# Performance work log

Measured on AMD Instinct MI355X. Metric: run time of the kernel, lower is better.

## Reference

```python
import jax, jax.numpy as jnp
import numpy as np

D_MODEL = 1024
NHEAD = 16
HEAD_DIM = D_MODEL // NHEAD


def setup_inputs() -> dict:
    key = jax.random.key(0)
    ks = jax.random.split(key, 11)
    B, S = 4, 2048
    s = 1.0 / np.sqrt(D_MODEL)
    return {
        "q": jax.random.normal(ks[0], (B, S, D_MODEL), jnp.float32),
        "k": jax.random.normal(ks[1], (B, S, D_MODEL), jnp.float32),
        "v": jax.random.normal(ks[2], (B, S, D_MODEL), jnp.float32),
        "Wq": jax.random.normal(ks[3], (D_MODEL, D_MODEL), jnp.float32) * s,
        "bq": jnp.zeros((D_MODEL,), jnp.float32),
        "Wk": jax.random.normal(ks[4], (D_MODEL, D_MODEL), jnp.float32) * s,
        "bk": jnp.zeros((D_MODEL,), jnp.float32),
        "Wv": jax.random.normal(ks[5], (D_MODEL, D_MODEL), jnp.float32) * s,
        "bv": jnp.zeros((D_MODEL,), jnp.float32),
        "Wo": jax.random.normal(ks[6], (D_MODEL, D_MODEL), jnp.float32) * s,
        "bo": jnp.zeros((D_MODEL,), jnp.float32),
    }


def reference(q, k, v, Wq, bq, Wk, bk, Wv, bv, Wo, bo):
    B, S, _ = q.shape
    H, Dh = NHEAD, HEAD_DIM

    def proj(x, W, b):  # nn.Linear: x @ W.T + b, then split heads -> [B,H,S,Dh]
        y = x @ W.T + b
        return y.reshape(B, S, H, Dh).transpose(0, 2, 1, 3)

    qh = proj(q, Wq, bq)
    kh = proj(k, Wk, bk)
    vh = proj(v, Wv, bv)

    scores = jnp.einsum("bhsd,bhtd->bhst", qh, kh) / jnp.sqrt(jnp.float32(Dh))
    attn = jax.nn.softmax(scores, axis=-1)
    out = jnp.einsum("bhst,bhtd->bhsd", attn, vh)  # [B,H,S,Dh]
    out = out.transpose(0, 2, 1, 3).reshape(B, S, H * Dh)
    return out @ Wo.T + bo
```

## Files before the change

### kernel.cpp

```cpp
#include <hip/hip_runtime.h>


typedef short bf16x8 __attribute__((ext_vector_type(8)));
typedef short bf16x4 __attribute__((ext_vector_type(4)));
typedef float f32x4 __attribute__((ext_vector_type(4)));
typedef float f32x16 __attribute__((ext_vector_type(16)));
typedef unsigned int u32x4 __attribute__((ext_vector_type(4)));

__device__ __forceinline__ short f2bf(float x) {
    union { float f; unsigned int u; } un; un.f = x;
    unsigned int u = un.u;
    return (short)(unsigned short)((u + 0x7fffu + ((u >> 16) & 1u)) >> 16);
}

__device__ __forceinline__ void gll16(const void* g, void* l) {
    __builtin_amdgcn_global_load_lds(
        (const __attribute__((address_space(1))) void*)g,
        (__attribute__((address_space(3))) void*)l, 16, 0, 0);
}

__device__ __forceinline__ void plswap(unsigned& a, unsigned& b) {
    asm("v_permlane32_swap_b32 %0, %1" : "+v"(a), "+v"(b));
}

struct CvtArgs { const float* s[4]; unsigned short* d[4]; int n4; };
__global__ __launch_bounds__(256) void cvt_bf16(CvtArgs ca) {
    const float* s = ca.s[blockIdx.y];
    unsigned short* d = ca.d[blockIdx.y];
    int i = blockIdx.x * blockDim.x + threadIdx.x;
    int stride = gridDim.x * blockDim.x;
    const float4* s4 = reinterpret_cast<const float4*>(s);
    bf16x4* d4 = reinterpret_cast<bf16x4*>(d);
    for (; i < ca.n4; i += stride) {
        float4 x = s4[i];
        bf16x4 y;
        y[0] = f2bf(x.x); y[1] = f2bf(x.y); y[2] = f2bf(x.z); y[3] = f2bf(x.w);
        d4[i] = y;
    }
}

__device__ __forceinline__ void gemm_core(const unsigned short* __restrict__ A,
                                          const unsigned short* __restrict__ W,
                                          const float* __restrict__ bias,
                                          float scale, void* __restrict__ out,
                                          int mode) {
    __shared__ unsigned short As[2][128 * 64];
    __shared__ unsigned short Bs[2][128 * 64];
    const int tid = threadIdx.x;
    const int m0 = blockIdx.y * 128, n0 = blockIdx.x * 128;
    const int wave = tid >> 6, lane = tid & 63;
    const int wm = (wave >> 1) * 64, wn = (wave & 1) * 64;
    const int l15 = lane & 15, quad = lane >> 4;
    const int srow = tid >> 3;
    const int scol = ((tid & 7) ^ (srow & 7)) * 8;
    const int cb = (l15 & 7);

    f32x4 acc[4][4] = {};

#pragma unroll
    for (int ro = 0; ro < 4; ++ro) {
        gll16(&A[(size_t)(m0 + ro * 32 + srow) * 1024 + scol], &As[0][ro * 2048 + tid * 8]);
        gll16(&W[(size_t)(n0 + ro * 32 + srow) * 1024 + scol], &Bs[0][ro * 2048 + tid * 8]);
    }
    __syncthreads();

    for (int kt = 0; kt < 16; ++kt) {
        const int cur = kt & 1;
        if (kt < 15) {
            const int k0 = (kt + 1) * 64;
#pragma unroll
            for (int ro = 0; ro < 4; ++ro) {
                gll16(&A[(size_t)(m0 + ro * 32 + srow) * 1024 + k0 + scol], &As[cur ^ 1][ro * 2048 + tid * 8]);
                gll16(&W[(size_t)(n0 + ro * 32 + srow) * 1024 + k0 + scol], &Bs[cur ^ 1][ro * 2048 + tid * 8]);
            }
        }
#pragma unroll
        for (int kk = 0; kk < 2; ++kk) {
            const int co = ((4 * kk + quad) ^ cb) * 8;
            bf16x8 a[4], b[4];
#pragma unroll
            for (int i = 0; i < 4; ++i)
                a[i] = *reinterpret_cast<bf16x8*>(&As[cur][(wm + i * 16 + l15) * 64 + co]);
#pragma unroll
            for (int j = 0; j < 4; ++j)
                b[j] = *reinterpret_cast<bf16x8*>(&Bs[cur][(wn + j * 16 + l15) * 64 + co]);
#pragma unroll
            for (int i = 0; i < 4; ++i)
#pragma unroll
                for (int j = 0; j < 4; ++j)
                    acc[i][j] = __builtin_amdgcn_mfma_f32_16x16x32_bf16(a[i], b[j], acc[i][j], 0, 0, 0);
        }
        __syncthreads();
    }

#pragma unroll
    for (int i = 0; i < 4; ++i) {
#pragma unroll
        for (int j = 0; j < 4; ++j) {
#pragma unroll
            for (int r = 0; r < 4; ++r) {
                int m = m0 + wm + i * 16 + quad * 4 + r;
                int n = n0 + wn + j * 16 + l15;
                float val = (acc[i][j][r] + bias[n]) * scale;
                if (mode == 0) {
                    reinterpret_cast<float*>(out)[(size_t)m * 1024 + n] = val;
                } else {
                    int b_ = m >> 11, s = m & 2047, h = n >> 6, d = n & 63;
                    size_t off = (mode == 1)
                                     ? ((size_t)((b_ * 16 + h) * 2048 + s) * 64 + d)
                                     : ((size_t)((b_ * 16 + h) * 64 + d) * 2048 + s);
                    reinterpret_cast<unsigned short*>(out)[off] = (unsigned short)f2bf(val);
                }
            }
        }
    }
}

struct QkvArgs {
    const unsigned short* A[3];
    const unsigned short* W[3];
    const float* bias[3];
    float scale[3];
    unsigned short* out[3];
    int mode[3];
};
__global__ __launch_bounds__(256) void gemm_qkv(QkvArgs ga) {
    int z = blockIdx.z;
    gemm_core(ga.A[z], ga.W[z], ga.bias[z], ga.scale[z], ga.out[z], ga.mode[z]);
}

__global__ __launch_bounds__(256) void gemm_wo(const unsigned short* __restrict__ A,
                                               const unsigned short* __restrict__ W,
                                               const float* __restrict__ bias,
                                               float* __restrict__ out) {
    gemm_core(A, W, bias, 1.0f, out, 0);
}


#define SOFTMAX_PV(MT, VBASE)                                                        \
    {                                                                                \
        float e[16];                                                                 \
        _Pragma("unroll")                                                            \
        for (int r = 0; r < 16; ++r) e[r] = __builtin_amdgcn_exp2f(sacc[MT][r]);     \
        lacc += ((e[0] + e[1]) + (e[2] + e[3])) + ((e[4] + e[5]) + (e[6] + e[7])) +  \
                ((e[8] + e[9]) + (e[10] + e[11])) + ((e[12] + e[13]) + (e[14] + e[15])); \
        unsigned w[8];                                                               \
        _Pragma("unroll")                                                            \
        for (int t = 0; t < 8; ++t) {                                                \
            union { float f; unsigned u; } a0{e[2 * t]}, a1{e[2 * t + 1]};           \
            w[t] = __builtin_amdgcn_perm(a1.u + 0x8000u, a0.u + 0x8000u, 0x07060302u); \
        }                                                                            \
        plswap(w[0], w[2]); plswap(w[1], w[3]);                                      \
        plswap(w[4], w[6]); plswap(w[5], w[7]);                                      \
        u32x4 t0; t0[0] = w[0]; t0[1] = w[1]; t0[2] = w[2]; t0[3] = w[3];            \
        u32x4 t1; t1[0] = w[4]; t1[1] = w[5]; t1[2] = w[6]; t1[3] = w[7];            \
        bf16x8 pa0 = __builtin_bit_cast(bf16x8, t0);                                 \
        bf16x8 pa1 = __builtin_bit_cast(bf16x8, t1);                                 \
        __builtin_amdgcn_s_setprio(1);                                               \
        _Pragma("unroll")                                                            \
        for (int nt = 0; nt < 2; ++nt) {                                             \
            bf16x8 bv0 = *reinterpret_cast<const bf16x8*>(&(VBASE)[rowoff[nt] + chx[2 * (MT)]]); \
            bf16x8 bv1 = *reinterpret_cast<const bf16x8*>(&(VBASE)[rowoff[nt] + chx[2 * (MT) + 1]]); \
            o[nt] = __builtin_amdgcn_mfma_f32_32x32x16_bf16(pa0, bv0, o[nt], 0, 0, 0); \
            o[nt] = __builtin_amdgcn_mfma_f32_32x32x16_bf16(pa1, bv1, o[nt], 0, 0, 0); \
        }                                                                            \
        __builtin_amdgcn_s_setprio(0);                                               \
    }

#define QK_TILE(KBASE)                                                               \
    {                                                                                \
        f32x16 zz = {};                                                              \
        sacc[0] = zz; sacc[1] = zz;                                                  \
        __builtin_amdgcn_s_setprio(1);                                               \
        _Pragma("unroll")                                                            \
        for (int c = 0; c < 4; ++c) {                                                \
            bf16x8 ak0 = *reinterpret_cast<const bf16x8*>(&(KBASE)[rowoff[0] + chx[c]]); \
            bf16x8 ak1 = *reinterpret_cast<const bf16x8*>(&(KBASE)[rowoff[1] + chx[c]]); \
            sacc[0] = __builtin_amdgcn_mfma_f32_32x32x16_bf16(ak0, qreg[c], sacc[0], 0, 0, 0); \
            sacc[1] = __builtin_amdgcn_mfma_f32_32x32x16_bf16(ak1, qreg[c], sacc[1], 0, 0, 0); \
        }                                                                            \
        __builtin_amdgcn_s_setprio(0);                                               \
    }

__global__ __launch_bounds__(256, 4) void flash_attn(const unsigned short* __restrict__ Qh,
                                                     const unsigned short* __restrict__ Kh,
                                                     const unsigned short* __restrict__ Vt,
                                                     unsigned short* __restrict__ Oa) {
    __shared__ unsigned short Ks[2][64 * 64];
    __shared__ unsigned short Vs[2][64 * 64];
    const int tid = threadIdx.x;
    const int bh = blockIdx.y;
    const int q0 = blockIdx.x * 128;
    const unsigned short* Qb = Qh + (size_t)bh * 2048 * 64;
    const unsigned short* Kb = Kh + (size_t)bh * 2048 * 64;
    const unsigned short* Vb = Vt + (size_t)bh * 64 * 2048;
    const int wave = tid >> 6, lane = tid & 63;
    const int l31 = lane & 31, hi = lane >> 5;
    const int wq = wave * 32;
    const int srow = tid >> 3;
    const int scol = ((tid & 7) ^ (srow & 7)) * 8;

    int chx[4], rowoff[2];
#pragma unroll
    for (int c = 0; c < 4; ++c) chx[c] = ((c * 2 + hi) ^ (l31 & 7)) * 8;
    rowoff[0] = l31 * 64;
    rowoff[1] = (32 + l31) * 64;

    bf16x8 qreg[4];
#pragma unroll
    for (int c = 0; c < 4; ++c)
        qreg[c] = *reinterpret_cast<const bf16x8*>(
            &Qb[(size_t)(q0 + wq + l31) * 64 + c * 16 + hi * 8]);

    f32x16 o[2] = {};
    f32x16 sacc[2];
    float lacc = 0.f;

#pragma unroll
    for (int ro = 0; ro < 2; ++ro) {
        gll16(&Kb[(size_t)(ro * 32 + srow) * 64 + scol], &Ks[0][ro * 2048 + tid * 8]);
        gll16(&Vb[(size_t)(ro * 32 + srow) * 2048 + scol], &Vs[0][ro * 2048 + tid * 8]);
        gll16(&Kb[(size_t)(64 + ro * 32 + srow) * 64 + scol], &Ks[1][ro * 2048 + tid * 8]);
    }
    __syncthreads();
    QK_TILE(Ks[0]);
    __syncthreads();

    for (int it = 0; it < 31; ++it) {
        const int cur = it & 1, nxt = cur ^ 1;
        if (it < 30) {
            const int kvn = (it + 2) * 64;
#pragma unroll
            for (int ro = 0; ro < 2; ++ro)
                gll16(&Kb[(size_t)(kvn + ro * 32 + srow) * 64 + scol], &Ks[cur][ro * 2048 + tid * 8]);
        }
        {
            const int kvn = (it + 1) * 64;
#pragma unroll
            for (int ro = 0; ro < 2; ++ro)
                gll16(&Vb[(size_t)(ro * 32 + srow) * 2048 + kvn + scol], &Vs[nxt][ro * 2048 + tid * 8]);
        }

        SOFTMAX_PV(0, Vs[cur]);
        SOFTMAX_PV(1, Vs[cur]);

        QK_TILE(Ks[nxt]);

        __syncthreads();
    }
    SOFTMAX_PV(0, Vs[1]);
    SOFTMAX_PV(1, Vs[1]);

    float lfull = lacc + __shfl_xor(lacc, 32, 64);
    float rinv = 1.0f / lfull;
    const int b_ = bh >> 4, h = bh & 15;
#pragma unroll
    for (int r = 0; r < 16; ++r) {
        const int qrow = (r & 3) + 8 * (r >> 2) + 4 * hi;
        const float rl = __shfl(rinv, qrow, 64);
        const int s = q0 + wq + qrow;
#pragma unroll
        for (int nt = 0; nt < 2; ++nt) {
            const int d = nt * 32 + l31;
            Oa[(size_t)(b_ * 2048 + s) * 1024 + h * 64 + d] =
                (unsigned short)f2bf(o[nt][r] * rl);
        }
    }
}

extern "C" void kernel_launch(void* const* d_in, const int* in_sizes, int n_in,
                              void* d_out, int out_size, void* d_ws, size_t ws_size,
                              hipStream_t stream) {
    const float* q  = (const float*)d_in[0];
    const float* k  = (const float*)d_in[1];
    const float* v  = (const float*)d_in[2];
    const float* Wq = (const float*)d_in[3];
    const float* bq = (const float*)d_in[4];
    const float* Wk = (const float*)d_in[5];
    const float* bk = (const float*)d_in[6];
    const float* Wv = (const float*)d_in[7];
    const float* bv = (const float*)d_in[8];
    const float* Wo = (const float*)d_in[9];
    const float* bo = (const float*)d_in[10];

    const size_t E = (size_t)8192 * 1024;
    const size_t WE = (size_t)1024 * 1024;
    unsigned short* r0 = (unsigned short*)d_ws;
    unsigned short* r1 = r0 + E;
    unsigned short* r2 = r1 + E;
    unsigned short* r3 = r2 + E;
    unsigned short* wqb = r3 + E;
    unsigned short* wkb = wqb + WE;
    unsigned short* wvb = wkb + WE;
    unsigned short* wob = wvb + WE;

    CvtArgs ca;
    ca.s[0] = q; ca.d[0] = r0;
    ca.s[1] = k; ca.d[1] = r1;
    ca.s[2] = v; ca.d[2] = r2;
    ca.s[3] = q; ca.d[3] = r0;
    ca.n4 = (int)(E / 4);
    cvt_bf16<<<dim3(1024, 3), 256, 0, stream>>>(ca);

    CvtArgs cw;
    cw.s[0] = Wq; cw.d[0] = wqb;
    cw.s[1] = Wk; cw.d[1] = wkb;
    cw.s[2] = Wv; cw.d[2] = wvb;
    cw.s[3] = Wo; cw.d[3] = wob;
    cw.n4 = (int)(WE / 4);
    cvt_bf16<<<dim3(256, 4), 256, 0, stream>>>(cw);

    const float QSCALE = 0.125f * 1.44269504088896340736f;

    QkvArgs ga;
    ga.A[0] = r0; ga.W[0] = wqb; ga.bias[0] = bq; ga.scale[0] = QSCALE; ga.out[0] = r3; ga.mode[0] = 1;
    ga.A[1] = r1; ga.W[1] = wkb; ga.bias[1] = bk; ga.scale[1] = 1.0f;   ga.out[1] = r0; ga.mode[1] = 1;
    ga.A[2] = r2; ga.W[2] = wvb; ga.bias[2] = bv; ga.scale[2] = 1.0f;   ga.out[2] = r1; ga.mode[2] = 2;
    gemm_qkv<<<dim3(8, 64, 3), 256, 0, stream>>>(ga);

    flash_attn<<<dim3(16, 64), 256, 0, stream>>>(r3, r0, r1, r2);
    gemm_wo<<<dim3(8, 64), 256, 0, stream>>>(r2, wob, bo, (float*)d_out);
}
```

Baseline: 368.6 us.

## Restructure projection GEMM to 128x256 tiles with triple-buffered LDS pipeline

```diff
diff --git a/kernel.cpp b/kernel.cpp
--- a/kernel.cpp
+++ b/kernel.cpp
@@ -22,6 +22,9 @@
 __device__ __forceinline__ void plswap(unsigned& a, unsigned& b) {
     asm("v_permlane32_swap_b32 %0, %1" : "+v"(a), "+v"(b));
 }
+
+#define SBAR()   asm volatile("s_barrier" ::: "memory")
+#define VMCNT6() asm volatile("s_waitcnt vmcnt(6)" ::: "memory")
 
 struct CvtArgs { const float* s[4]; unsigned short* d[4]; int n4; };
 __global__ __launch_bounds__(256) void cvt_bf16(CvtArgs ca) {
@@ -44,54 +47,97 @@
                                           const float* __restrict__ bias,
                                           float scale, void* __restrict__ out,
                                           int mode) {
-    __shared__ unsigned short As[2][128 * 64];
-    __shared__ unsigned short Bs[2][128 * 64];
+    __shared__ unsigned short As[3 * 128 * 64];
+    __shared__ unsigned short Bs[3 * 256 * 64];
     const int tid = threadIdx.x;
-    const int m0 = blockIdx.y * 128, n0 = blockIdx.x * 128;
+    const int orid = blockIdx.x + 4 * blockIdx.y;
+    const int swz = ((orid & 7) << 5) | (orid >> 3);
+    const int n0 = (swz & 3) * 256;
+    const int m0 = (swz >> 2) * 128;
     const int wave = tid >> 6, lane = tid & 63;
-    const int wm = (wave >> 1) * 64, wn = (wave & 1) * 64;
+    const int wmr = (wave >> 2) * 64, wnr = (wave & 3) * 64;
     const int l15 = lane & 15, quad = lane >> 4;
+    const int cb = l15 & 7;
     const int srow = tid >> 3;
     const int scol = ((tid & 7) ^ (srow & 7)) * 8;
-    const int cb = (l15 & 7);
 
     f32x4 acc[4][4] = {};
 
-#pragma unroll
-    for (int ro = 0; ro < 4; ++ro) {
-        gll16(&A[(size_t)(m0 + ro * 32 + srow) * 1024 + scol], &As[0][ro * 2048 + tid * 8]);
-        gll16(&W[(size_t)(n0 + ro * 32 + srow) * 1024 + scol], &Bs[0][ro * 2048 + tid * 8]);
-    }
-    __syncthreads();
-
+#define SA(kt, sl)                                                                  \
+    {                                                                               \
+        gll16(&A[(size_t)(m0 + srow) * 1024 + (kt) * 64 + scol],                    \
+              &As[(sl) * 8192 + tid * 8]);                                          \
+        gll16(&A[(size_t)(m0 + 64 + srow) * 1024 + (kt) * 64 + scol],               \
+              &As[(sl) * 8192 + 4096 + tid * 8]);                                   \
+    }
+#define SB(kt, sl, ro)                                                              \
+    gll16(&W[(size_t)(n0 + (ro) * 64 + srow) * 1024 + (kt) * 64 + scol],            \
+          &Bs[(sl) * 16384 + (ro) * 4096 + tid * 8]);
+
+    SA(0, 0); SB(0, 0, 0); SB(0, 0, 1); SB(0, 0, 2); SB(0, 0, 3);
+    SA(1, 1); SB(1, 1, 0); SB(1, 1, 1); SB(1, 1, 2); SB(1, 1, 3);
+    VMCNT6();
+    __builtin_amdgcn_sched_barrier(0);
+    SBAR();
+    __builtin_amdgcn_sched_barrier(0);
+
+    int sl = 0;
     for (int kt = 0; kt < 16; ++kt) {
-        const int cur = kt & 1;
-        if (kt < 15) {
-            const int k0 = (kt + 1) * 64;
-#pragma unroll
-            for (int ro = 0; ro < 4; ++ro) {
-                gll16(&A[(size_t)(m0 + ro * 32 + srow) * 1024 + k0 + scol], &As[cur ^ 1][ro * 2048 + tid * 8]);
-                gll16(&W[(size_t)(n0 + ro * 32 + srow) * 1024 + k0 + scol], &Bs[cur ^ 1][ro * 2048 + tid * 8]);
-            }
-        }
-#pragma unroll
-        for (int kk = 0; kk < 2; ++kk) {
-            const int co = ((4 * kk + quad) ^ cb) * 8;
+        const int ss = (sl + 2 >= 3) ? sl - 1 : sl + 2;
+        const unsigned short* Ab = &As[sl * 8192];
+        const unsigned short* Bb = &Bs[sl * 16384];
+        {
+            const int co = (quad ^ cb) * 8;
             bf16x8 a[4], b[4];
 #pragma unroll
             for (int i = 0; i < 4; ++i)
-                a[i] = *reinterpret_cast<bf16x8*>(&As[cur][(wm + i * 16 + l15) * 64 + co]);
+                a[i] = *reinterpret_cast<const bf16x8*>(&Ab[(wmr + i * 16 + l15) * 64 + co]);
 #pragma unroll
             for (int j = 0; j < 4; ++j)
-                b[j] = *reinterpret_cast<bf16x8*>(&Bs[cur][(wn + j * 16 + l15) * 64 + co]);
+                b[j] = *reinterpret_cast<const bf16x8*>(&Bb[(wnr + j * 16 + l15) * 64 + co]);
+            if (kt < 14) { SA(kt + 2, ss); SB(kt + 2, ss, 0); }
+            SBAR();
+            __builtin_amdgcn_sched_barrier(0);
+            __builtin_amdgcn_s_setprio(1);
 #pragma unroll
             for (int i = 0; i < 4; ++i)
 #pragma unroll
                 for (int j = 0; j < 4; ++j)
                     acc[i][j] = __builtin_amdgcn_mfma_f32_16x16x32_bf16(a[i], b[j], acc[i][j], 0, 0, 0);
-        }
-        __syncthreads();
-    }
+            __builtin_amdgcn_s_setprio(0);
+            SBAR();
+            __builtin_amdgcn_sched_barrier(0);
+        }
+        {
+            const int co = ((4 + quad) ^ cb) * 8;
+            bf16x8 a[4], b[4];
+#pragma unroll
+            for (int i = 0; i < 4; ++i)
+                a[i] = *reinterpret_cast<const bf16x8*>(&Ab[(wmr + i * 16 + l15) * 64 + co]);
+#pragma unroll
+            for (int j = 0; j < 4; ++j)
+                b[j] = *reinterpret_cast<const bf16x8*>(&Bb[(wnr + j * 16 + l15) * 64 + co]);
+            if (kt < 14) { SB(kt + 2, ss, 1); SB(kt + 2, ss, 2); SB(kt + 2, ss, 3); }
+            if (kt < 15) {
+                VMCNT6();
+                __builtin_amdgcn_sched_barrier(0);
+            }
+            SBAR();
+            __builtin_amdgcn_sched_barrier(0);
+            __builtin_amdgcn_s_setprio(1);
+#pragma unroll
+            for (int i = 0; i < 4; ++i)
+#pragma unroll
+                for (int j = 0; j < 4; ++j)
+                    acc[i][j] = __builtin_amdgcn_mfma_f32_16x16x32_bf16(a[i], b[j], acc[i][j], 0, 0, 0);
+            __builtin_amdgcn_s_setprio(0);
+            SBAR();
+            __builtin_amdgcn_sched_barrier(0);
+        }
+        sl = (sl + 1 == 3) ? 0 : sl + 1;
+    }
+#undef SA
+#undef SB
 
 #pragma unroll
     for (int i = 0; i < 4; ++i) {
@@ -99,8 +145,8 @@
         for (int j = 0; j < 4; ++j) {
 #pragma unroll
             for (int r = 0; r < 4; ++r) {
-                int m = m0 + wm + i * 16 + quad * 4 + r;
-                int n = n0 + wn + j * 16 + l15;
+                int m = m0 + wmr + i * 16 + quad * 4 + r;
+                int n = n0 + wnr + j * 16 + l15;
                 float val = (acc[i][j][r] + bias[n]) * scale;
                 if (mode == 0) {
                     reinterpret_cast<float*>(out)[(size_t)m * 1024 + n] = val;
@@ -124,15 +170,15 @@
     unsigned short* out[3];
     int mode[3];
 };
-__global__ __launch_bounds__(256) void gemm_qkv(QkvArgs ga) {
+__global__ __launch_bounds__(512, 2) void gemm_qkv(QkvArgs ga) {
     int z = blockIdx.z;
     gemm_core(ga.A[z], ga.W[z], ga.bias[z], ga.scale[z], ga.out[z], ga.mode[z]);
 }
 
-__global__ __launch_bounds__(256) void gemm_wo(const unsigned short* __restrict__ A,
-                                               const unsigned short* __restrict__ W,
-                                               const float* __restrict__ bias,
-                                               float* __restrict__ out) {
+__global__ __launch_bounds__(512, 2) void gemm_wo(const unsigned short* __restrict__ A,
+                                                  const unsigned short* __restrict__ W,
+                                                  const float* __restrict__ bias,
+                                                  float* __restrict__ out) {
     gemm_core(A, W, bias, 1.0f, out, 0);
 }
 
@@ -316,8 +362,8 @@
     ga.A[0] = r0; ga.W[0] = wqb; ga.bias[0] = bq; ga.scale[0] = QSCALE; ga.out[0] = r3; ga.mode[0] = 1;
     ga.A[1] = r1; ga.W[1] = wkb; ga.bias[1] = bk; ga.scale[1] = 1.0f;   ga.out[1] = r0; ga.mode[1] = 1;
     ga.A[2] = r2; ga.W[2] = wvb; ga.bias[2] = bv; ga.scale[2] = 1.0f;   ga.out[2] = r1; ga.mode[2] = 2;
-    gemm_qkv<<<dim3(8, 64, 3), 256, 0, stream>>>(ga);
+    gemm_qkv<<<dim3(4, 64, 3), 512, 0, stream>>>(ga);
 
     flash_attn<<<dim3(16, 64), 256, 0, stream>>>(r3, r0, r1, r2);
-    gemm_wo<<<dim3(8, 64), 256, 0, stream>>>(r2, wob, bo, (float*)d_out);
-}
+    gemm_wo<<<dim3(4, 64), 512, 0, stream>>>(r2, wob, bo, (float*)d_out);
+}
```

After: 349.7 us. 1.05x faster.

## Fuse fp32-to-bf16 conversion into GEMM tile loads and drop separate cvt kernels

Applied to the files above, without the earlier changes.

```diff
diff --git a/kernel.cpp b/kernel.cpp
--- a/kernel.cpp
+++ b/kernel.cpp
@@ -23,56 +23,85 @@
     asm("v_permlane32_swap_b32 %0, %1" : "+v"(a), "+v"(b));
 }
 
-struct CvtArgs { const float* s[4]; unsigned short* d[4]; int n4; };
-__global__ __launch_bounds__(256) void cvt_bf16(CvtArgs ca) {
-    const float* s = ca.s[blockIdx.y];
-    unsigned short* d = ca.d[blockIdx.y];
-    int i = blockIdx.x * blockDim.x + threadIdx.x;
-    int stride = gridDim.x * blockDim.x;
-    const float4* s4 = reinterpret_cast<const float4*>(s);
-    bf16x4* d4 = reinterpret_cast<bf16x4*>(d);
-    for (; i < ca.n4; i += stride) {
-        float4 x = s4[i];
-        bf16x4 y;
-        y[0] = f2bf(x.x); y[1] = f2bf(x.y); y[2] = f2bf(x.z); y[3] = f2bf(x.w);
-        d4[i] = y;
-    }
-}
-
-__device__ __forceinline__ void gemm_core(const unsigned short* __restrict__ A,
-                                          const unsigned short* __restrict__ W,
+__device__ __forceinline__ unsigned cvtpk(float lo, float hi) {
+    unsigned r;
+    asm("v_cvt_pk_bf16_f32 %0, %1, %2" : "=v"(r) : "v"(lo), "v"(hi));
+    return r;
+}
+
+__device__ __forceinline__ bf16x8 cvt8(float4 a, float4 b) {
+    u32x4 r;
+    r[0] = cvtpk(a.x, a.y);
+    r[1] = cvtpk(a.z, a.w);
+    r[2] = cvtpk(b.x, b.y);
+    r[3] = cvtpk(b.z, b.w);
+    return __builtin_bit_cast(bf16x8, r);
+}
+
+template <bool AF32>
+__device__ __forceinline__ void gemm_core(const void* __restrict__ Ap,
+                                          const float* __restrict__ Wf,
                                           const float* __restrict__ bias,
                                           float scale, void* __restrict__ out,
                                           int mode) {
     __shared__ unsigned short As[2][128 * 64];
     __shared__ unsigned short Bs[2][128 * 64];
     const int tid = threadIdx.x;
-    const int m0 = blockIdx.y * 128, n0 = blockIdx.x * 128;
+    const int orid = blockIdx.x + 8 * blockIdx.y;
+    const int swz = ((orid & 7) << 6) | (orid >> 3);
+    const int n0 = (swz & 7) * 128;
+    const int m0 = (swz >> 3) * 128;
     const int wave = tid >> 6, lane = tid & 63;
     const int wm = (wave >> 1) * 64, wn = (wave & 1) * 64;
     const int l15 = lane & 15, quad = lane >> 4;
     const int srow = tid >> 3;
     const int scol = ((tid & 7) ^ (srow & 7)) * 8;
-    const int cb = (l15 & 7);
+    const int cb = l15 & 7;
+
+    const float4* A4 = reinterpret_cast<const float4*>(Ap);
+    const unsigned short* Ab = reinterpret_cast<const unsigned short*>(Ap);
+    const float4* W4 = reinterpret_cast<const float4*>(Wf);
 
     f32x4 acc[4][4] = {};
-
-#pragma unroll
-    for (int ro = 0; ro < 4; ++ro) {
-        gll16(&A[(size_t)(m0 + ro * 32 + srow) * 1024 + scol], &As[0][ro * 2048 + tid * 8]);
-        gll16(&W[(size_t)(n0 + ro * 32 + srow) * 1024 + scol], &Bs[0][ro * 2048 + tid * 8]);
-    }
+    float4 pa[4][2], pw[4][2];
+
+#define ISSUE_AF32(k0)                                                              \
+    _Pragma("unroll")                                                               \
+    for (int ro = 0; ro < 4; ++ro) {                                                \
+        size_t ix = (size_t)(m0 + ro * 32 + srow) * 256 + ((k0) + scol) / 4;        \
+        pa[ro][0] = A4[ix]; pa[ro][1] = A4[ix + 1];                                 \
+    }
+#define ISSUE_ABF16(k0, b)                                                          \
+    _Pragma("unroll")                                                               \
+    for (int ro = 0; ro < 4; ++ro)                                                  \
+        gll16(&Ab[(size_t)(m0 + ro * 32 + srow) * 1024 + (k0) + scol],              \
+              &As[b][ro * 2048 + tid * 8]);
+#define ISSUE_W(k0)                                                                 \
+    _Pragma("unroll")                                                               \
+    for (int ro = 0; ro < 4; ++ro) {                                                \
+        size_t ix = (size_t)(n0 + ro * 32 + srow) * 256 + ((k0) + scol) / 4;        \
+        pw[ro][0] = W4[ix]; pw[ro][1] = W4[ix + 1];                                 \
+    }
+#define WRITE_A(b)                                                                  \
+    _Pragma("unroll")                                                               \
+    for (int ro = 0; ro < 4; ++ro)                                                  \
+        *reinterpret_cast<bf16x8*>(&As[b][ro * 2048 + tid * 8]) = cvt8(pa[ro][0], pa[ro][1]);
+#define WRITE_W(b)                                                                  \
+    _Pragma("unroll")                                                               \
+    for (int ro = 0; ro < 4; ++ro)                                                  \
+        *reinterpret_cast<bf16x8*>(&Bs[b][ro * 2048 + tid * 8]) = cvt8(pw[ro][0], pw[ro][1]);
+
+    if constexpr (AF32) { ISSUE_AF32(0); } else { ISSUE_ABF16(0, 0); }
+    ISSUE_W(0);
+    if constexpr (AF32) { WRITE_A(0); }
+    WRITE_W(0);
     __syncthreads();
 
     for (int kt = 0; kt < 16; ++kt) {
         const int cur = kt & 1;
         if (kt < 15) {
-            const int k0 = (kt + 1) * 64;
-#pragma unroll
-            for (int ro = 0; ro < 4; ++ro) {
-                gll16(&A[(size_t)(m0 + ro * 32 + srow) * 1024 + k0 + scol], &As[cur ^ 1][ro * 2048 + tid * 8]);
-                gll16(&W[(size_t)(n0 + ro * 32 + srow) * 1024 + k0 + scol], &Bs[cur ^ 1][ro * 2048 + tid * 8]);
-            }
+            if constexpr (AF32) { ISSUE_AF32((kt + 1) * 64); } else { ISSUE_ABF16((kt + 1) * 64, cur ^ 1); }
+            ISSUE_W((kt + 1) * 64);
         }
 #pragma unroll
         for (int kk = 0; kk < 2; ++kk) {
@@ -90,8 +119,17 @@
                 for (int j = 0; j < 4; ++j)
                     acc[i][j] = __builtin_amdgcn_mfma_f32_16x16x32_bf16(a[i], b[j], acc[i][j], 0, 0, 0);
         }
+        if (kt < 15) {
+            if constexpr (AF32) { WRITE_A(cur ^ 1); }
+            WRITE_W(cur ^ 1);
+        }
         __syncthreads();
     }
+#undef ISSUE_AF32
+#undef ISSUE_ABF16
+#undef ISSUE_W
+#undef WRITE_A
+#undef WRITE_W
 
 #pragma unroll
     for (int i = 0; i < 4; ++i) {
@@ -117,23 +155,23 @@
 }
 
 struct QkvArgs {
-    const unsigned short* A[3];
-    const unsigned short* W[3];
+    const float* A[3];
+    const float* W[3];
     const float* bias[3];
     float scale[3];
     unsigned short* out[3];
     int mode[3];
 };
-__global__ __launch_bounds__(256) void gemm_qkv(QkvArgs ga) {
+__global__ __launch_bounds__(256, 2) void gemm_qkv(QkvArgs ga) {
     int z = blockIdx.z;
-    gemm_core(ga.A[z], ga.W[z], ga.bias[z], ga.scale[z], ga.out[z], ga.mode[z]);
-}
-
-__global__ __launch_bounds__(256) void gemm_wo(const unsigned short* __restrict__ A,
-                                               const unsigned short* __restrict__ W,
-                                               const float* __restrict__ bias,
-                                               float* __restrict__ out) {
-    gemm_core(A, W, bias, 1.0f, out, 0);
+    gemm_core<true>(ga.A[z], ga.W[z], ga.bias[z], ga.scale[z], ga.out[z], ga.mode[z]);
+}
+
+__global__ __launch_bounds__(256, 2) void gemm_wo(const unsigned short* __restrict__ A,
+                                                  const float* __restrict__ W,
+                                                  const float* __restrict__ bias,
+                                                  float* __restrict__ out) {
+    gemm_core<false>(A, W, bias, 1.0f, out, 0);
 }
 
 
@@ -284,40 +322,19 @@
     const float* bo = (const float*)d_in[10];
 
     const size_t E = (size_t)8192 * 1024;
-    const size_t WE = (size_t)1024 * 1024;
     unsigned short* r0 = (unsigned short*)d_ws;
     unsigned short* r1 = r0 + E;
     unsigned short* r2 = r1 + E;
     unsigned short* r3 = r2 + E;
-    unsigned short* wqb = r3 + E;
-    unsigned short* wkb = wqb + WE;
-    unsigned short* wvb = wkb + WE;
-    unsigned short* wob = wvb + WE;
-
-    CvtArgs ca;
-    ca.s[0] = q; ca.d[0] = r0;
-    ca.s[1] = k; ca.d[1] = r1;
-    ca.s[2] = v; ca.d[2] = r2;
-    ca.s[3] = q; ca.d[3] = r0;
-    ca.n4 = (int)(E / 4);
-    cvt_bf16<<<dim3(1024, 3), 256, 0, stream>>>(ca);
-
-    CvtArgs cw;
-    cw.s[0] = Wq; cw.d[0] = wqb;
-    cw.s[1] = Wk; cw.d[1] = wkb;
-    cw.s[2] = Wv; cw.d[2] = wvb;
-    cw.s[3] = Wo; cw.d[3] = wob;
-    cw.n4 = (int)(WE / 4);
-    cvt_bf16<<<dim3(256, 4), 256, 0, stream>>>(cw);
 
     const float QSCALE = 0.125f * 1.44269504088896340736f;
 
     QkvArgs ga;
-    ga.A[0] = r0; ga.W[0] = wqb; ga.bias[0] = bq; ga.scale[0] = QSCALE; ga.out[0] = r3; ga.mode[0] = 1;
-    ga.A[1] = r1; ga.W[1] = wkb; ga.bias[1] = bk; ga.scale[1] = 1.0f;   ga.out[1] = r0; ga.mode[1] = 1;
-    ga.A[2] = r2; ga.W[2] = wvb; ga.bias[2] = bv; ga.scale[2] = 1.0f;   ga.out[2] = r1; ga.mode[2] = 2;
+    ga.A[0] = q; ga.W[0] = Wq; ga.bias[0] = bq; ga.scale[0] = QSCALE; ga.out[0] = r3; ga.mode[0] = 1;
+    ga.A[1] = k; ga.W[1] = Wk; ga.bias[1] = bk; ga.scale[1] = 1.0f;   ga.out[1] = r0; ga.mode[1] = 1;
+    ga.A[2] = v; ga.W[2] = Wv; ga.bias[2] = bv; ga.scale[2] = 1.0f;   ga.out[2] = r1; ga.mode[2] = 2;
     gemm_qkv<<<dim3(8, 64, 3), 256, 0, stream>>>(ga);
 
     flash_attn<<<dim3(16, 64), 256, 0, stream>>>(r3, r0, r1, r2);
-    gemm_wo<<<dim3(8, 64), 256, 0, stream>>>(r2, wob, bo, (float*)d_out);
-}
+    gemm_wo<<<dim3(8, 64), 256, 0, stream>>>(r2, Wo, bo, (float*)d_out);
+}
```

New measurement: 385.5 us. 4.6% more time.
